# Optimization experiments

Measured on AMD Instinct MI355X. Metric: run time of the kernel, lower is better.

The kernel has to match this reference:

```python
import jax, jax.numpy as jnp
import numpy as np
import math

D_MODEL = 1024
N_HEADS = 16
D_K = D_MODEL // N_HEADS
D_FF = 4096
B, S = 2, 1024
EPS = 1e-6
MASK_FILL = 1e-9  # source uses masked_fill_(mask==0, 1e-09), NOT -inf


def layer_norm(x, alpha, bias):
    # torch: mean + unbiased std (ddof=1), normalized by (std + eps)
    mean = jnp.mean(x, axis=-1, keepdims=True)
    std = jnp.std(x, axis=-1, keepdims=True, ddof=1)
    return alpha * (x - mean) / (std + EPS) + bias


def setup_inputs() -> dict:
    key = jax.random.key(0)
    ks = jax.random.split(key, 6)
    sc = 0.02
    return {
        "x": jax.random.normal(ks[0], (B, S, D_MODEL), jnp.float32),
        "mask": jax.random.randint(ks[1], (B, 1, S, S), 0, 2, jnp.int32),
        "Wq": jax.random.normal(ks[2], (D_MODEL, D_MODEL), jnp.float32) * sc,
        "Wo": jax.random.normal(ks[3], (D_MODEL, D_MODEL), jnp.float32) * sc,
        "W1": jax.random.normal(ks[4], (D_MODEL, D_FF), jnp.float32) * sc,
        "B1": jnp.zeros((D_FF,), jnp.float32),
        "W2": jax.random.normal(ks[5], (D_FF, D_MODEL), jnp.float32) * sc,
        "B2": jnp.zeros((D_MODEL,), jnp.float32),
        "ln1_a": jnp.ones((D_MODEL,), jnp.float32),
        "ln1_b": jnp.zeros((D_MODEL,), jnp.float32),
        "ln2_a": jnp.ones((D_MODEL,), jnp.float32),
        "ln2_b": jnp.zeros((D_MODEL,), jnp.float32),
    }


def reference(x, mask, Wq, Wo, W1, B1, W2, B2, ln1_a, ln1_b, ln2_a, ln2_b):
    # --- residual 1: pre-norm self-attention ---
    n = layer_norm(x, ln1_a, ln1_b)
    # source bug preserved: Wq is applied to q, k AND v; q==k==v here
    qkv = (n @ Wq).reshape(B, S, N_HEADS, D_K).transpose(0, 2, 1, 3)  # [B,H,S,dk]
    scores = jnp.einsum('bhqd,bhkd->bhqk', qkv, qkv) / math.sqrt(D_K)
    scores = jnp.where(mask == 0, MASK_FILL, scores)
    attn = jax.nn.softmax(scores, axis=-1)
    ctx = jnp.einsum('bhqk,bhkd->bhqd', attn, qkv)
    ctx = ctx.transpose(0, 2, 1, 3).reshape(B, S, D_MODEL)
    x = x + ctx @ Wo
    # --- residual 2: pre-norm FFN ---
    n2 = layer_norm(x, ln2_a, ln2_b)
    ff = jax.nn.relu(n2 @ W1 + B1) @ W2 + B2
    return x + ff
```

## Files before the change

kernel.cpp:

```cpp
#include <hip/hip_runtime.h>
#include <hip/hip_bf16.h>
#include <stdint.h>

#define D_MODEL 1024
#define S_LEN 1024
#define BATCH 2
#define NHEADS 16
#define DK 64
#define DFF 4096

typedef __attribute__((ext_vector_type(8))) short short8;
typedef __attribute__((ext_vector_type(4))) float f32x4;

__device__ __forceinline__ unsigned short f2bf(float f) {
  union { float f; unsigned u; } v; v.f = f;
  unsigned r = v.u + 0x7FFFu + ((v.u >> 16) & 1u);
  return (unsigned short)(r >> 16);
}

__device__ __forceinline__ float bf2f(unsigned short s) {
  union { float f; unsigned u; } v; v.u = ((unsigned)s) << 16;
  return v.f;
}

__device__ __forceinline__ void gll16(const void* g, void* l) {
  __builtin_amdgcn_global_load_lds(
      (const __attribute__((address_space(1))) void*)g,
      (__attribute__((address_space(3))) void*)l, 16, 0, 0);
}

__global__ __launch_bounds__(256)
void ln_kernel(const float* __restrict__ x,
               const float* __restrict__ alpha,
               const float* __restrict__ beta,
               unsigned short* __restrict__ out) {
  const int row = blockIdx.x;
  const int tid = threadIdx.x;
  const float4 v = ((const float4*)(x + (int64_t)row * D_MODEL))[tid];
  float s = v.x + v.y + v.z + v.w;
  float ss = v.x * v.x + v.y * v.y + v.z * v.z + v.w * v.w;
  #pragma unroll
  for (int m = 32; m; m >>= 1) {
    s += __shfl_down(s, m);
    ss += __shfl_down(ss, m);
  }
  __shared__ float red[10];
  const int wave = tid >> 6;
  if ((tid & 63) == 0) { red[wave] = s; red[4 + wave] = ss; }
  __syncthreads();
  if (tid == 0) {
    float S = red[0] + red[1] + red[2] + red[3];
    float SS = red[4] + red[5] + red[6] + red[7];
    float mean = S * (1.f / 1024.f);
    float var = (SS - 1024.f * mean * mean) * (1.f / 1023.f);
    float inv = 1.f / (sqrtf(fmaxf(var, 0.f)) + 1e-6f);
    red[8] = mean; red[9] = inv;
  }
  __syncthreads();
  const float mean = red[8], inv = red[9];
  const float4 a = ((const float4*)alpha)[tid];
  const float4 bb = ((const float4*)beta)[tid];
  union { unsigned short us[4]; uint2 u2; } pk;
  pk.us[0] = f2bf(a.x * (v.x - mean) * inv + bb.x);
  pk.us[1] = f2bf(a.y * (v.y - mean) * inv + bb.y);
  pk.us[2] = f2bf(a.z * (v.z - mean) * inv + bb.z);
  pk.us[3] = f2bf(a.w * (v.w - mean) * inv + bb.w);
  ((uint2*)(out + (int64_t)row * D_MODEL))[tid] = pk.u2;
}

__global__ __launch_bounds__(256)
void wt_kernel(const float* __restrict__ W, unsigned short* __restrict__ Wt,
               int K, int N) {
  __shared__ unsigned short tile[32][33];
  const int k0 = blockIdx.y * 32, n0 = blockIdx.x * 32;
  const int tx = threadIdx.x & 31, ty = threadIdx.x >> 5;
  #pragma unroll
  for (int i = 0; i < 4; i++) {
    int r = ty + i * 8;
    tile[r][tx] = f2bf(W[(int64_t)(k0 + r) * N + n0 + tx]);
  }
  __syncthreads();
  #pragma unroll
  for (int i = 0; i < 4; i++) {
    int r = ty + i * 8;
    Wt[(int64_t)(n0 + r) * K + k0 + tx] = tile[tx][r];
  }
}

__global__ __launch_bounds__(256)
void qkvt_kernel(const unsigned short* __restrict__ qkv,
                 unsigned short* __restrict__ qkvT) {
  __shared__ unsigned short tile[32][33];
  const int s0 = blockIdx.x * 32, d0 = blockIdx.y * 32, bh = blockIdx.z;
  const int b = bh >> 4, h = bh & 15;
  const int tx = threadIdx.x & 31, ty = threadIdx.x >> 5;
  #pragma unroll
  for (int i = 0; i < 4; i++) {
    int r = ty + i * 8;
    tile[r][tx] = qkv[(int64_t)(b * S_LEN + s0 + r) * D_MODEL + h * DK + d0 + tx];
  }
  __syncthreads();
  #pragma unroll
  for (int i = 0; i < 4; i++) {
    int r = ty + i * 8;
    qkvT[(int64_t)(bh * DK + d0 + r) * S_LEN + s0 + tx] = tile[tx][r];
  }
}

__global__ __launch_bounds__(256)
void mprep_kernel(const int* __restrict__ mask, unsigned short* __restrict__ Mf) {
  const int gid = blockIdx.x * 256 + threadIdx.x;
  const int lo = gid & 15;
  const int ktb = (gid >> 4) & 31;
  const int q4 = (gid >> 9) & 255;
  const int b = gid >> 17;
  const int* mrow = mask + ((int64_t)b << 20) + (int64_t)q4 * 4096 + ktb * 32 + lo;
  union { unsigned short us[8]; short8 v; } o;
  #pragma unroll
  for (int r = 0; r < 4; r++) {
    o.us[r * 2]     = mrow[r * 1024]      ? 0x3F80 : 0;
    o.us[r * 2 + 1] = mrow[r * 1024 + 16] ? 0x3F80 : 0;
  }
  ((short8*)Mf)[gid] = o.v;
}

template<int BM, int BN, int BK, int BIAS, int RELU, int RES, int OUTBF>
__global__ __launch_bounds__(256)
void gemm_t(const unsigned short* __restrict__ A,
            const unsigned short* __restrict__ Bt,
            const float* __restrict__ bias,
            const float* __restrict__ res,
            void* __restrict__ outp,
            int M, int N, int K) {
  constexpr int NCH = BK / 8;
  constexpr int RPW = 512 / BK;
  constexpr int RPR = 2048 / BK;
  constexpr int RA = (BM * BK) / 2048;
  constexpr int RB = (BN * BK) / 2048;
  constexpr int MI = BM / 32;
  constexpr int NJ = BN / 32;
  constexpr int KK = BK / 32;

  __shared__ __align__(16) unsigned short As[BM * BK];
  __shared__ __align__(16) unsigned short Bs[BN * BK];

  const int tid = threadIdx.x;
  const int lane = tid & 63;
  const int wave = tid >> 6;
  const int lo = lane & 15, hi = lane >> 4;

  const int cpx = gridDim.x >> 3;
  const int sid = (blockIdx.x & 7) * cpx + (blockIdx.x >> 3);
  const int nbx = N / BN;
  const int n0 = (sid % nbx) * BN;
  const int m0 = (sid / nbx) * BM;
  const int wr = (wave >> 1) * (BM / 2);
  const int wc = (wave & 1) * (BN / 2);

  auto swz = [](int row, int c) -> int {
    if (BK == 128) return c ^ ((row & 7) << 1);
    if (BK == 64)  return c ^ (row & 7);
    return c ^ ((row >> 1) & 3);
  };

  const int sr = lane / NCH;
  const int sc = lane % NCH;

  f32x4 acc[MI][NJ] = {};

  for (int k0 = 0; k0 < K; k0 += BK) {
    #pragma unroll
    for (int r = 0; r < RA; r++) {
      const int row = r * RPR + wave * RPW + sr;
      gll16(A + (int64_t)(m0 + row) * K + k0 + swz(row, sc) * 8,
            &As[r * 2048 + wave * 512]);
    }
    #pragma unroll
    for (int r = 0; r < RB; r++) {
      const int row = r * RPR + wave * RPW + sr;
      gll16(Bt + (int64_t)(n0 + row) * K + k0 + swz(row, sc) * 8,
            &Bs[r * 2048 + wave * 512]);
    }
    __syncthreads();
    #pragma unroll
    for (int kk = 0; kk < KK; kk++) {
      short8 af[MI], bfr[NJ];
      #pragma unroll
      for (int t = 0; t < MI; t++) {
        const int row = wr + t * 16 + lo;
        af[t] = *(const short8*)&As[row * BK + swz(row, kk * 4 + hi) * 8];
      }
      #pragma unroll
      for (int t = 0; t < NJ; t++) {
        const int row = wc + t * 16 + lo;
        bfr[t] = *(const short8*)&Bs[row * BK + swz(row, kk * 4 + hi) * 8];
      }
      #pragma unroll
      for (int i = 0; i < MI; i++)
        #pragma unroll
        for (int j = 0; j < NJ; j++)
          acc[i][j] = __builtin_amdgcn_mfma_f32_16x16x32_bf16(af[i], bfr[j], acc[i][j], 0, 0, 0);
    }
    __syncthreads();
  }

  #pragma unroll
  for (int i = 0; i < MI; i++) {
    const int row = m0 + wr + i * 16 + hi * 4;
    #pragma unroll
    for (int j = 0; j < NJ; j++) {
      const int col = n0 + wc + j * 16 + lo;
      #pragma unroll
      for (int r = 0; r < 4; r++) {
        float v = acc[i][j][r];
        if (BIAS) v += bias[col];
        if (RELU) v = fmaxf(v, 0.f);
        if (RES)  v += res[(int64_t)(row + r) * N + col];
        if (OUTBF)
          ((unsigned short*)outp)[(int64_t)(row + r) * N + col] = f2bf(v);
        else
          ((float*)outp)[(int64_t)(row + r) * N + col] = v;
      }
    }
  }
}

__global__ __launch_bounds__(256)
void attn_kernel(const unsigned short* __restrict__ qkv,
                 const unsigned short* __restrict__ qkvT,
                 const unsigned short* __restrict__ Mf,
                 float* __restrict__ part,
                 float* __restrict__ psum) {
  __shared__ __align__(16) unsigned short Ks[64 * 64];
  __shared__ __align__(16) unsigned short Vs[64 * 64];
  __shared__ __align__(16) unsigned short Ms[512 * 8];
  __shared__ __align__(16) unsigned short Plds[4][16 * 40];
  const int tid = threadIdx.x;
  const int lane = tid & 63;
  const int wave = tid >> 6;
  const int lo = lane & 15, hi = lane >> 4;
  const int L = blockIdx.x;
  const int xcd = L & 7, idx = L >> 3;
  const int b = xcd >> 2;
  const int h = (xcd & 3) * 4 + (idx >> 5);
  const int split = (idx >> 4) & 1;
  const int qt = idx & 15;
  const int bh = b * 16 + h;
  const int q0 = qt * 64 + wave * 16;

  const unsigned short* qb =
      qkv + (int64_t)(b * S_LEN + q0 + lo) * D_MODEL + h * DK + hi * 8;
  const short8 qf0 = *(const short8*)qb;
  const short8 qf1 = *(const short8*)(qb + 32);

  f32x4 oacc[4] = {};
  float rsum[4] = {0.f, 0.f, 0.f, 0.f};
  unsigned short* Pw = Plds[wave];
  const int kbeg = split * 512;
  const int q4w = wave * 4 + hi;
  const int xr = lo & 7;

  for (int kti = 0; kti < 8; kti++) {
    const int kt = kbeg + kti * 64;
    #pragma unroll
    for (int r = 0; r < 2; r++) {
      const int c = r * 256 + tid;
      const int row = c >> 3;
      const int chg = (c & 7) ^ (row & 7);
      gll16(qkv + (int64_t)(b * S_LEN + kt + row) * D_MODEL + h * DK + chg * 8,
            &Ks[(r * 256 + wave * 64) * 8]);
      gll16(qkvT + (int64_t)(bh * DK + row) * S_LEN + kt + chg * 8,
            &Vs[(r * 256 + wave * 64) * 8]);
      const int q4l = c >> 5;
      const int u2 = (c >> 4) & 1;
      const int log = (c & 15) ^ q4l;
      gll16(Mf + ((int64_t)((b * 256 + qt * 16 + q4l) * 32 + (kt >> 5) + u2) * 16 + log) * 8,
            &Ms[(r * 256 + wave * 64) * 8]);
    }
    __syncthreads();
    #pragma unroll
    for (int u = 0; u < 2; u++) {
      const short8 kf00 = *(const short8*)&Ks[((u * 32 + lo) * 8 + (hi ^ xr)) * 8];
      const short8 kf01 = *(const short8*)&Ks[((u * 32 + lo) * 8 + ((4 + hi) ^ xr)) * 8];
      const short8 kf10 = *(const short8*)&Ks[((u * 32 + 16 + lo) * 8 + (hi ^ xr)) * 8];
      const short8 kf11 = *(const short8*)&Ks[((u * 32 + 16 + lo) * 8 + ((4 + hi) ^ xr)) * 8];
      const short8 mf = *(const short8*)&Ms[(q4w * 32 + u * 16 + (lo ^ q4w)) * 8];
      f32x4 s0 = {}, s1 = {};
      s0 = __builtin_amdgcn_mfma_f32_16x16x32_bf16(qf0, kf00, s0, 0, 0, 0);
      s0 = __builtin_amdgcn_mfma_f32_16x16x32_bf16(qf1, kf01, s0, 0, 0, 0);
      s1 = __builtin_amdgcn_mfma_f32_16x16x32_bf16(qf0, kf10, s1, 0, 0, 0);
      s1 = __builtin_amdgcn_mfma_f32_16x16x32_bf16(qf1, kf11, s1, 0, 0, 0);
      #pragma unroll
      for (int r = 0; r < 4; r++) {
        const float m0_ = bf2f((unsigned short)mf[r * 2]);
        const float m1_ = bf2f((unsigned short)mf[r * 2 + 1]);
        const float e0_ = __expf(s0[r] * 0.125f);
        const float e1_ = __expf(s1[r] * 0.125f);
        const float p0_ = fmaf(m0_, e0_ - 1.f, 1.f);
        const float p1_ = fmaf(m1_, e1_ - 1.f, 1.f);
        rsum[r] += p0_ + p1_;
        Pw[(hi * 4 + r) * 40 + lo]      = f2bf(p0_);
        Pw[(hi * 4 + r) * 40 + 16 + lo] = f2bf(p1_);
      }
      const short8 pf = *(const short8*)&Pw[lo * 40 + hi * 8];
      #pragma unroll
      for (int t = 0; t < 4; t++) {
        const short8 vf = *(const short8*)&Vs[((t * 16 + lo) * 8 + ((u * 4 + hi) ^ xr)) * 8];
        oacc[t] = __builtin_amdgcn_mfma_f32_16x16x32_bf16(pf, vf, oacc[t], 0, 0, 0);
      }
    }
    __syncthreads();
  }

  #pragma unroll
  for (int m = 1; m < 16; m <<= 1)
    #pragma unroll
    for (int r = 0; r < 4; r++) rsum[r] += __shfl_xor(rsum[r], m);

  const int64_t prow = (int64_t)(split * 32 + bh) * 1024;
  #pragma unroll
  for (int t = 0; t < 4; t++)
    #pragma unroll
    for (int r = 0; r < 4; r++)
      part[(prow + q0 + hi * 4 + r) * 64 + t * 16 + lo] = oacc[t][r];
  if (lo == 0)
    #pragma unroll
    for (int r = 0; r < 4; r++)
      psum[prow + q0 + hi * 4 + r] = rsum[r];
}

__global__ __launch_bounds__(256)
void acomb_kernel(const float* __restrict__ part,
                  const float* __restrict__ psum,
                  unsigned short* __restrict__ ctx) {
  const int idx4 = blockIdx.x * 256 + threadIdx.x;
  const int d4 = idx4 & 15;
  const int q = (idx4 >> 4) & 1023;
  const int bh = idx4 >> 14;
  const int b = bh >> 4, h = bh & 15;
  const float4* p4 = (const float4*)part;
  const float4 a0 = p4[(int64_t)(bh * 1024 + q) * 16 + d4];
  const float4 a1 = p4[524288 + (int64_t)(bh * 1024 + q) * 16 + d4];
  const float rs = psum[bh * 1024 + q] + psum[32768 + bh * 1024 + q];
  const float inv = 1.f / rs;
  union { unsigned short us[4]; uint2 u2; } pk;
  pk.us[0] = f2bf((a0.x + a1.x) * inv);
  pk.us[1] = f2bf((a0.y + a1.y) * inv);
  pk.us[2] = f2bf((a0.z + a1.z) * inv);
  pk.us[3] = f2bf((a0.w + a1.w) * inv);
  *(uint2*)(ctx + (int64_t)(b * S_LEN + q) * D_MODEL + h * DK + d4 * 4) = pk.u2;
}

extern "C" void kernel_launch(void* const* d_in, const int* in_sizes, int n_in,
                              void* d_out, int out_size, void* d_ws, size_t ws_size,
                              hipStream_t stream) {
  (void)in_sizes; (void)n_in; (void)out_size; (void)ws_size;
  const float* x    = (const float*)d_in[0];
  const int*   mask = (const int*)d_in[1];
  const float* Wq   = (const float*)d_in[2];
  const float* Wo   = (const float*)d_in[3];
  const float* W1   = (const float*)d_in[4];
  const float* B1   = (const float*)d_in[5];
  const float* W2   = (const float*)d_in[6];
  const float* B2   = (const float*)d_in[7];
  const float* ln1a = (const float*)d_in[8];
  const float* ln1b = (const float*)d_in[9];
  const float* ln2a = (const float*)d_in[10];
  const float* ln2b = (const float*)d_in[11];
  float* out = (float*)d_out;

  char* ws = (char*)d_ws;
  unsigned short* WqT  = (unsigned short*)(ws);
  unsigned short* WoT  = (unsigned short*)(ws + (2ull  << 20));
  unsigned short* W1T  = (unsigned short*)(ws + (4ull  << 20));
  unsigned short* W2T  = (unsigned short*)(ws + (12ull << 20));
  unsigned short* n1   = (unsigned short*)(ws + (20ull << 20));
  float*          psum = (float*)(ws + (20ull << 20));
  unsigned short* qkv  = (unsigned short*)(ws + (24ull << 20));
  unsigned short* qkvT = (unsigned short*)(ws + (28ull << 20));
  unsigned short* Mf   = (unsigned short*)(ws + (32ull << 20));
  unsigned short* ctx  = (unsigned short*)(ws + (32ull << 20));
  unsigned short* n2   = (unsigned short*)(ws + (36ull << 20));
  float*          part = (float*)(ws + (40ull << 20));
  unsigned short* h1   = (unsigned short*)(ws + (40ull << 20));
  float* x1 = out;

  dim3 blk(256);
  wt_kernel<<<dim3(32, 32),  blk, 0, stream>>>(Wq, WqT, 1024, 1024);
  wt_kernel<<<dim3(32, 32),  blk, 0, stream>>>(Wo, WoT, 1024, 1024);
  wt_kernel<<<dim3(128, 32), blk, 0, stream>>>(W1, W1T, 1024, 4096);
  wt_kernel<<<dim3(32, 128), blk, 0, stream>>>(W2, W2T, 4096, 1024);
  mprep_kernel<<<1024, blk, 0, stream>>>(mask, Mf);

  ln_kernel<<<2048, blk, 0, stream>>>(x, ln1a, ln1b, n1);
  gemm_t<64,64,128, 0,0,0,1><<<512, blk, 0, stream>>>(n1, WqT, nullptr, nullptr, qkv, 2048, 1024, 1024);
  qkvt_kernel<<<dim3(32, 2, 32), blk, 0, stream>>>(qkv, qkvT);
  attn_kernel<<<1024, blk, 0, stream>>>(qkv, qkvT, Mf, part, psum);
  acomb_kernel<<<2048, blk, 0, stream>>>(part, psum, ctx);
  gemm_t<64,64,128, 0,0,1,0><<<512, blk, 0, stream>>>(ctx, WoT, nullptr, x, x1, 2048, 1024, 1024);
  ln_kernel<<<2048, blk, 0, stream>>>(x1, ln2a, ln2b, n2);
  gemm_t<128,128,64, 1,1,0,1><<<512, blk, 0, stream>>>(n2, W1T, B1, nullptr, h1, 2048, 4096, 1024);
  gemm_t<64,64,128, 1,0,1,0><<<512, blk, 0, stream>>>(h1, W2T, B2, x1, out, 2048, 1024, 4096);
}
```

Measured before the change: 145.2 us.

## Double-buffer GEMM loads, split K across waves, merge weight transposes

Replaces the templated GEMM with a double-buffered variant that prefetches the next K tile during compute. For the 64x64 GEMMs each wave takes a different 32-wide K slice of the 128-wide tile, and the per-wave partial sums are combined through LDS before the epilogue. A specialized FFN1 GEMM keeps the 128x128 tile with double buffering. The four weight-transpose launches are merged into one. This aims to hide global-load latency and cut launch overhead, at the cost of doubled LDS use (lower occupancy) and an extra cross-wave reduction.

Result: slower. 495.5 us (+241.3%).

```diff
diff --git a/kernel.cpp b/kernel.cpp
--- a/kernel.cpp
+++ b/kernel.cpp
@@ -69,10 +69,18 @@
 }
 
 __global__ __launch_bounds__(256)
-void wt_kernel(const float* __restrict__ W, unsigned short* __restrict__ Wt,
-               int K, int N) {
+void wtall_kernel(const float* __restrict__ Wq, const float* __restrict__ Wo,
+                  const float* __restrict__ W1, const float* __restrict__ W2,
+                  unsigned short* __restrict__ WqT, unsigned short* __restrict__ WoT,
+                  unsigned short* __restrict__ W1T, unsigned short* __restrict__ W2T) {
   __shared__ unsigned short tile[32][33];
-  const int k0 = blockIdx.y * 32, n0 = blockIdx.x * 32;
+  int id = blockIdx.x;
+  const float* W; unsigned short* Wt; int K, N, bx, by;
+  if (id < 1024)      { W = Wq; Wt = WqT; K = 1024; N = 1024; bx = id & 31;  by = id >> 5; }
+  else if (id < 2048) { id -= 1024; W = Wo; Wt = WoT; K = 1024; N = 1024; bx = id & 31;  by = id >> 5; }
+  else if (id < 6144) { id -= 2048; W = W1; Wt = W1T; K = 1024; N = 4096; bx = id & 127; by = id >> 7; }
+  else                { id -= 6144; W = W2; Wt = W2T; K = 4096; N = 1024; bx = id & 31;  by = id >> 5; }
+  const int k0 = by * 32, n0 = bx * 32;
   const int tx = threadIdx.x & 31, ty = threadIdx.x >> 5;
   #pragma unroll
   for (int i = 0; i < 4; i++) {
@@ -124,26 +132,16 @@
   ((short8*)Mf)[gid] = o.v;
 }
 
-template<int BM, int BN, int BK, int BIAS, int RELU, int RES, int OUTBF>
-__global__ __launch_bounds__(256)
-void gemm_t(const unsigned short* __restrict__ A,
-            const unsigned short* __restrict__ Bt,
-            const float* __restrict__ bias,
-            const float* __restrict__ res,
-            void* __restrict__ outp,
-            int M, int N, int K) {
-  constexpr int NCH = BK / 8;
-  constexpr int RPW = 512 / BK;
-  constexpr int RPR = 2048 / BK;
-  constexpr int RA = (BM * BK) / 2048;
-  constexpr int RB = (BN * BK) / 2048;
-  constexpr int MI = BM / 32;
-  constexpr int NJ = BN / 32;
-  constexpr int KK = BK / 32;
-
-  __shared__ __align__(16) unsigned short As[BM * BK];
-  __shared__ __align__(16) unsigned short Bs[BN * BK];
-
+template<int BIAS, int RELU, int RES, int OUTBF>
+__global__ __launch_bounds__(256)
+void gemm_ks(const unsigned short* __restrict__ A,
+             const unsigned short* __restrict__ Bt,
+             const float* __restrict__ bias,
+             const float* __restrict__ res,
+             void* __restrict__ outp,
+             int M, int N, int K) {
+  __shared__ __align__(16) unsigned short As[2][8192];
+  __shared__ __align__(16) unsigned short Bs[2][8192];
   const int tid = threadIdx.x;
   const int lane = tid & 63;
   const int wave = tid >> 6;
@@ -151,75 +149,187 @@
 
   const int cpx = gridDim.x >> 3;
   const int sid = (blockIdx.x & 7) * cpx + (blockIdx.x >> 3);
-  const int nbx = N / BN;
-  const int n0 = (sid % nbx) * BN;
-  const int m0 = (sid / nbx) * BM;
-  const int wr = (wave >> 1) * (BM / 2);
-  const int wc = (wave & 1) * (BN / 2);
-
-  auto swz = [](int row, int c) -> int {
-    if (BK == 128) return c ^ ((row & 7) << 1);
-    if (BK == 64)  return c ^ (row & 7);
-    return c ^ ((row >> 1) & 3);
+  const int nbx = N >> 6;
+  const int n0 = (sid % nbx) << 6;
+  const int m0 = (sid / nbx) << 6;
+
+  const int sr = lane >> 4;
+  const int sc = lane & 15;
+  const int srow = wave * 4 + sr;
+  const int sch = (sc ^ (srow & 7)) * 8;
+  const unsigned short* Ag = A + (int64_t)(m0 + srow) * K + sch;
+  const unsigned short* Bg = Bt + (int64_t)(n0 + srow) * K + sch;
+
+  const int rch = ((wave * 4 + hi) ^ (lo & 7)) * 8;
+
+  f32x4 acc[4][4] = {};
+  const int NT = K >> 7;
+
+  auto stage = [&](int buf, int k0) {
+    #pragma unroll
+    for (int r = 0; r < 4; r++)
+      gll16(Ag + (int64_t)r * 16 * K + k0, &As[buf][r * 2048 + wave * 512]);
+    #pragma unroll
+    for (int r = 0; r < 4; r++)
+      gll16(Bg + (int64_t)r * 16 * K + k0, &Bs[buf][r * 2048 + wave * 512]);
   };
 
-  const int sr = lane / NCH;
-  const int sc = lane % NCH;
-
-  f32x4 acc[MI][NJ] = {};
-
-  for (int k0 = 0; k0 < K; k0 += BK) {
-    #pragma unroll
-    for (int r = 0; r < RA; r++) {
-      const int row = r * RPR + wave * RPW + sr;
-      gll16(A + (int64_t)(m0 + row) * K + k0 + swz(row, sc) * 8,
-            &As[r * 2048 + wave * 512]);
+  stage(0, 0);
+  __syncthreads();
+  int cur = 0;
+  for (int t = 0; t < NT; t++) {
+    if (t + 1 < NT) stage(cur ^ 1, (t + 1) << 7);
+    short8 af[4], bf[4];
+    #pragma unroll
+    for (int q = 0; q < 4; q++) {
+      af[q] = *(const short8*)&As[cur][(q * 16 + lo) * 128 + rch];
+      bf[q] = *(const short8*)&Bs[cur][(q * 16 + lo) * 128 + rch];
     }
     #pragma unroll
-    for (int r = 0; r < RB; r++) {
-      const int row = r * RPR + wave * RPW + sr;
-      gll16(Bt + (int64_t)(n0 + row) * K + k0 + swz(row, sc) * 8,
-            &Bs[r * 2048 + wave * 512]);
+    for (int i = 0; i < 4; i++)
+      #pragma unroll
+      for (int j = 0; j < 4; j++)
+        acc[i][j] = __builtin_amdgcn_mfma_f32_16x16x32_bf16(af[i], bf[j], acc[i][j], 0, 0, 0);
+    __syncthreads();
+    cur ^= 1;
+  }
+
+  float* red = (float*)&As[0][0];
+  if (wave >= 2) {
+    #pragma unroll
+    for (int i = 0; i < 4; i++)
+      #pragma unroll
+      for (int j = 0; j < 4; j++)
+        *(f32x4*)&red[(wave - 2) * 4096 + (i * 4 + j) * 256 + lane * 4] = acc[i][j];
+  }
+  __syncthreads();
+  if (wave < 2) {
+    #pragma unroll
+    for (int i = 0; i < 4; i++)
+      #pragma unroll
+      for (int j = 0; j < 4; j++)
+        acc[i][j] += *(const f32x4*)&red[wave * 4096 + (i * 4 + j) * 256 + lane * 4];
+  }
+  __syncthreads();
+  if (wave == 0) {
+    #pragma unroll
+    for (int i = 2; i < 4; i++)
+      #pragma unroll
+      for (int j = 0; j < 4; j++)
+        *(f32x4*)&red[((i - 2) * 4 + j) * 256 + lane * 4] = acc[i][j];
+  } else if (wave == 1) {
+    #pragma unroll
+    for (int i = 0; i < 2; i++)
+      #pragma unroll
+      for (int j = 0; j < 4; j++)
+        *(f32x4*)&red[2048 + (i * 4 + j) * 256 + lane * 4] = acc[i][j];
+  }
+  __syncthreads();
+
+  if (wave < 2) {
+    const int ib = wave * 2;
+    #pragma unroll
+    for (int ii = 0; ii < 2; ii++) {
+      const int i = ib + ii;
+      #pragma unroll
+      for (int j = 0; j < 4; j++) {
+        f32x4 v4 = acc[i][j];
+        v4 += *(const f32x4*)&red[(wave ? (ii * 4 + j) * 256 : 2048 + (i * 4 + j) * 256) + lane * 4];
+        const int row = m0 + i * 16 + hi * 4;
+        const int col = n0 + j * 16 + lo;
+        #pragma unroll
+        for (int r = 0; r < 4; r++) {
+          float v = v4[r];
+          if (BIAS) v += bias[col];
+          if (RELU) v = fmaxf(v, 0.f);
+          if (RES)  v += res[(int64_t)(row + r) * N + col];
+          if (OUTBF)
+            ((unsigned short*)outp)[(int64_t)(row + r) * N + col] = f2bf(v);
+          else
+            ((float*)outp)[(int64_t)(row + r) * N + col] = v;
+        }
+      }
+    }
+  }
+}
+
+__global__ __launch_bounds__(256)
+void gemm_ffn1(const unsigned short* __restrict__ A,
+               const unsigned short* __restrict__ Bt,
+               const float* __restrict__ bias,
+               unsigned short* __restrict__ outp,
+               int M, int N, int K) {
+  __shared__ __align__(16) unsigned short As[2][8192];
+  __shared__ __align__(16) unsigned short Bs[2][8192];
+  const int tid = threadIdx.x;
+  const int lane = tid & 63;
+  const int wave = tid >> 6;
+  const int lo = lane & 15, hi = lane >> 4;
+
+  const int cpx = gridDim.x >> 3;
+  const int sid = (blockIdx.x & 7) * cpx + (blockIdx.x >> 3);
+  const int nbx = N >> 7;
+  const int n0 = (sid % nbx) << 7;
+  const int m0 = (sid / nbx) << 7;
+  const int wr = (wave >> 1) * 64;
+  const int wc = (wave & 1) * 64;
+
+  const int sr = lane >> 3;
+  const int sc = lane & 7;
+  const int srow = wave * 8 + sr;
+  const int sch = (sc ^ (srow & 7)) * 8;
+  const unsigned short* Ag = A + (int64_t)(m0 + srow) * K + sch;
+  const unsigned short* Bg = Bt + (int64_t)(n0 + srow) * K + sch;
+
+  const int xr = lo & 7;
+
+  f32x4 acc[4][4] = {};
+  const int NT = K >> 6;
+
+  auto stage = [&](int buf, int k0) {
+    #pragma unroll
+    for (int r = 0; r < 4; r++)
+      gll16(Ag + (int64_t)r * 32 * K + k0, &As[buf][r * 2048 + wave * 512]);
+    #pragma unroll
+    for (int r = 0; r < 4; r++)
+      gll16(Bg + (int64_t)r * 32 * K + k0, &Bs[buf][r * 2048 + wave * 512]);
+  };
+
+  stage(0, 0);
+  __syncthreads();
+  int cur = 0;
+  for (int t = 0; t < NT; t++) {
+    if (t + 1 < NT) stage(cur ^ 1, (t + 1) << 6);
+    #pragma unroll
+    for (int kk = 0; kk < 2; kk++) {
+      short8 af[4], bf[4];
+      const int ch = ((kk * 4 + hi) ^ xr) * 8;
+      #pragma unroll
+      for (int q = 0; q < 4; q++) {
+        af[q] = *(const short8*)&As[cur][(wr + q * 16 + lo) * 64 + ch];
+        bf[q] = *(const short8*)&Bs[cur][(wc + q * 16 + lo) * 64 + ch];
+      }
+      #pragma unroll
+      for (int i = 0; i < 4; i++)
+        #pragma unroll
+        for (int j = 0; j < 4; j++)
+          acc[i][j] = __builtin_amdgcn_mfma_f32_16x16x32_bf16(af[i], bf[j], acc[i][j], 0, 0, 0);
     }
     __syncthreads();
-    #pragma unroll
-    for (int kk = 0; kk < KK; kk++) {
-      short8 af[MI], bfr[NJ];
-      #pragma unroll
-      for (int t = 0; t < MI; t++) {
-        const int row = wr + t * 16 + lo;
-        af[t] = *(const short8*)&As[row * BK + swz(row, kk * 4 + hi) * 8];
-      }
-      #pragma unroll
-      for (int t = 0; t < NJ; t++) {
-        const int row = wc + t * 16 + lo;
-        bfr[t] = *(const short8*)&Bs[row * BK + swz(row, kk * 4 + hi) * 8];
-      }
-      #pragma unroll
-      for (int i = 0; i < MI; i++)
-        #pragma unroll
-        for (int j = 0; j < NJ; j++)
-          acc[i][j] = __builtin_amdgcn_mfma_f32_16x16x32_bf16(af[i], bfr[j], acc[i][j], 0, 0, 0);
-    }
-    __syncthreads();
-  }
-
-  #pragma unroll
-  for (int i = 0; i < MI; i++) {
+    cur ^= 1;
+  }
+
+  #pragma unroll
+  for (int i = 0; i < 4; i++) {
     const int row = m0 + wr + i * 16 + hi * 4;
     #pragma unroll
-    for (int j = 0; j < NJ; j++) {
+    for (int j = 0; j < 4; j++) {
       const int col = n0 + wc + j * 16 + lo;
+      const float bv = bias[col];
       #pragma unroll
       for (int r = 0; r < 4; r++) {
-        float v = acc[i][j][r];
-        if (BIAS) v += bias[col];
-        if (RELU) v = fmaxf(v, 0.f);
-        if (RES)  v += res[(int64_t)(row + r) * N + col];
-        if (OUTBF)
-          ((unsigned short*)outp)[(int64_t)(row + r) * N + col] = f2bf(v);
-        else
-          ((float*)outp)[(int64_t)(row + r) * N + col] = v;
+        float v = fmaxf(acc[i][j][r] + bv, 0.f);
+        outp[(int64_t)(row + r) * N + col] = f2bf(v);
       }
     }
   }
@@ -386,19 +496,16 @@
   float* x1 = out;
 
   dim3 blk(256);
-  wt_kernel<<<dim3(32, 32),  blk, 0, stream>>>(Wq, WqT, 1024, 1024);
-  wt_kernel<<<dim3(32, 32),  blk, 0, stream>>>(Wo, WoT, 1024, 1024);
-  wt_kernel<<<dim3(128, 32), blk, 0, stream>>>(W1, W1T, 1024, 4096);
-  wt_kernel<<<dim3(32, 128), blk, 0, stream>>>(W2, W2T, 4096, 1024);
+  wtall_kernel<<<10240, blk, 0, stream>>>(Wq, Wo, W1, W2, WqT, WoT, W1T, W2T);
   mprep_kernel<<<1024, blk, 0, stream>>>(mask, Mf);
 
   ln_kernel<<<2048, blk, 0, stream>>>(x, ln1a, ln1b, n1);
-  gemm_t<64,64,128, 0,0,0,1><<<512, blk, 0, stream>>>(n1, WqT, nullptr, nullptr, qkv, 2048, 1024, 1024);
+  gemm_ks<0,0,0,1><<<512, blk, 0, stream>>>(n1, WqT, nullptr, nullptr, qkv, 2048, 1024, 1024);
   qkvt_kernel<<<dim3(32, 2, 32), blk, 0, stream>>>(qkv, qkvT);
   attn_kernel<<<1024, blk, 0, stream>>>(qkv, qkvT, Mf, part, psum);
   acomb_kernel<<<2048, blk, 0, stream>>>(part, psum, ctx);
-  gemm_t<64,64,128, 0,0,1,0><<<512, blk, 0, stream>>>(ctx, WoT, nullptr, x, x1, 2048, 1024, 1024);
+  gemm_ks<0,0,1,0><<<512, blk, 0, stream>>>(ctx, WoT, nullptr, x, x1, 2048, 1024, 1024);
   ln_kernel<<<2048, blk, 0, stream>>>(x1, ln2a, ln2b, n2);
-  gemm_t<128,128,64, 1,1,0,1><<<512, blk, 0, stream>>>(n2, W1T, B1, nullptr, h1, 2048, 4096, 1024);
-  gemm_t<64,64,128, 1,0,1,0><<<512, blk, 0, stream>>>(h1, W2T, B2, x1, out, 2048, 1024, 4096);
-}
+  gemm_ffn1<<<512, blk, 0, stream>>>(n2, W1T, B1, h1, 2048, 4096, 1024);
+  gemm_ks<1,0,1,0><<<512, blk, 0, stream>>>(h1, W2T, B2, x1, out, 2048, 1024, 4096);
+}
```

## Double-buffer GEMM shared-memory tiles and merge weight transposes into one launch

Applied to the files above, without the earlier changes.

The GEMM kernel now uses two LDS buffers, issuing the global-to-LDS loads for the next K tile while MFMAs run on the current one, so there is one barrier per tile instead of two. BK is halved for each GEMM so LDS use stays roughly the same, and the load-address math is precomputed per thread. The four weight-transpose launches become one kernel that picks its matrix from the block index, which cuts launch overhead. The smaller BK doubles the number of loop iterations and barriers, and the unrolled pair loop assumes an even tile count.

After: 166.1 us. 1.14x slower.

```diff
diff --git a/kernel.cpp b/kernel.cpp
--- a/kernel.cpp
+++ b/kernel.cpp
@@ -69,10 +69,18 @@
 }
 
 __global__ __launch_bounds__(256)
-void wt_kernel(const float* __restrict__ W, unsigned short* __restrict__ Wt,
-               int K, int N) {
+void wtall_kernel(const float* __restrict__ Wq, const float* __restrict__ Wo,
+                  const float* __restrict__ W1, const float* __restrict__ W2,
+                  unsigned short* __restrict__ WqT, unsigned short* __restrict__ WoT,
+                  unsigned short* __restrict__ W1T, unsigned short* __restrict__ W2T) {
   __shared__ unsigned short tile[32][33];
-  const int k0 = blockIdx.y * 32, n0 = blockIdx.x * 32;
+  int id = blockIdx.x;
+  const float* W; unsigned short* Wt; int K, N, bx, by;
+  if (id < 1024)      { W = Wq; Wt = WqT; K = 1024; N = 1024; bx = id & 31;  by = id >> 5; }
+  else if (id < 2048) { id -= 1024; W = Wo; Wt = WoT; K = 1024; N = 1024; bx = id & 31;  by = id >> 5; }
+  else if (id < 6144) { id -= 2048; W = W1; Wt = W1T; K = 1024; N = 4096; bx = id & 127; by = id >> 7; }
+  else                { id -= 6144; W = W2; Wt = W2T; K = 4096; N = 1024; bx = id & 31;  by = id >> 5; }
+  const int k0 = by * 32, n0 = bx * 32;
   const int tx = threadIdx.x & 31, ty = threadIdx.x >> 5;
   #pragma unroll
   for (int i = 0; i < 4; i++) {
@@ -126,23 +134,21 @@
 
 template<int BM, int BN, int BK, int BIAS, int RELU, int RES, int OUTBF>
 __global__ __launch_bounds__(256)
-void gemm_t(const unsigned short* __restrict__ A,
-            const unsigned short* __restrict__ Bt,
-            const float* __restrict__ bias,
-            const float* __restrict__ res,
-            void* __restrict__ outp,
-            int M, int N, int K) {
+void gemm_db(const unsigned short* __restrict__ A,
+             const unsigned short* __restrict__ Bt,
+             const float* __restrict__ bias,
+             const float* __restrict__ res,
+             void* __restrict__ outp,
+             int M, int N, int K) {
   constexpr int NCH = BK / 8;
-  constexpr int RPW = 512 / BK;
-  constexpr int RPR = 2048 / BK;
   constexpr int RA = (BM * BK) / 2048;
   constexpr int RB = (BN * BK) / 2048;
   constexpr int MI = BM / 32;
   constexpr int NJ = BN / 32;
   constexpr int KK = BK / 32;
 
-  __shared__ __align__(16) unsigned short As[BM * BK];
-  __shared__ __align__(16) unsigned short Bs[BN * BK];
+  __shared__ __align__(16) unsigned short As[2][BM * BK];
+  __shared__ __align__(16) unsigned short Bs[2][BN * BK];
 
   const int tid = threadIdx.x;
   const int lane = tid & 63;
@@ -158,49 +164,70 @@
   const int wc = (wave & 1) * (BN / 2);
 
   auto swz = [](int row, int c) -> int {
-    if (BK == 128) return c ^ ((row & 7) << 1);
-    if (BK == 64)  return c ^ (row & 7);
+    if (BK >= 64) return c ^ (row & 7);
     return c ^ ((row >> 1) & 3);
   };
 
-  const int sr = lane / NCH;
-  const int sc = lane % NCH;
+  const unsigned short* Ap[RA];
+  const unsigned short* Bp[RB];
+  #pragma unroll
+  for (int r = 0; r < RA; r++) {
+    const int c = r * 256 + tid;
+    const int row = c / NCH, sc = c % NCH;
+    Ap[r] = A + (int64_t)(m0 + row) * K + swz(row, sc) * 8;
+  }
+  #pragma unroll
+  for (int r = 0; r < RB; r++) {
+    const int c = r * 256 + tid;
+    const int row = c / NCH, sc = c % NCH;
+    Bp[r] = Bt + (int64_t)(n0 + row) * K + swz(row, sc) * 8;
+  }
 
   f32x4 acc[MI][NJ] = {};
-
-  for (int k0 = 0; k0 < K; k0 += BK) {
-    #pragma unroll
-    for (int r = 0; r < RA; r++) {
-      const int row = r * RPR + wave * RPW + sr;
-      gll16(A + (int64_t)(m0 + row) * K + k0 + swz(row, sc) * 8,
-            &As[r * 2048 + wave * 512]);
-    }
-    #pragma unroll
-    for (int r = 0; r < RB; r++) {
-      const int row = r * RPR + wave * RPW + sr;
-      gll16(Bt + (int64_t)(n0 + row) * K + k0 + swz(row, sc) * 8,
-            &Bs[r * 2048 + wave * 512]);
-    }
-    __syncthreads();
+  const int NT = K / BK;
+
+  auto stage = [&](unsigned short* Al, unsigned short* Bl, int k0) {
+    #pragma unroll
+    for (int r = 0; r < RA; r++)
+      gll16(Ap[r] + k0, Al + (r * 256 + wave * 64) * 8);
+    #pragma unroll
+    for (int r = 0; r < RB; r++)
+      gll16(Bp[r] + k0, Bl + (r * 256 + wave * 64) * 8);
+  };
+
+  auto compute = [&](const unsigned short* Al, const unsigned short* Bl) {
     #pragma unroll
     for (int kk = 0; kk < KK; kk++) {
-      short8 af[MI], bfr[NJ];
+      short8 af[MI], bf[NJ];
       #pragma unroll
       for (int t = 0; t < MI; t++) {
         const int row = wr + t * 16 + lo;
-        af[t] = *(const short8*)&As[row * BK + swz(row, kk * 4 + hi) * 8];
+        af[t] = *(const short8*)&Al[row * BK + swz(row, kk * 4 + hi) * 8];
       }
       #pragma unroll
       for (int t = 0; t < NJ; t++) {
         const int row = wc + t * 16 + lo;
-        bfr[t] = *(const short8*)&Bs[row * BK + swz(row, kk * 4 + hi) * 8];
+        bf[t] = *(const short8*)&Bl[row * BK + swz(row, kk * 4 + hi) * 8];
       }
       #pragma unroll
       for (int i = 0; i < MI; i++)
         #pragma unroll
         for (int j = 0; j < NJ; j++)
-          acc[i][j] = __builtin_amdgcn_mfma_f32_16x16x32_bf16(af[i], bfr[j], acc[i][j], 0, 0, 0);
+          acc[i][j] = __builtin_amdgcn_mfma_f32_16x16x32_bf16(af[i], bf[j], acc[i][j], 0, 0, 0);
     }
+  };
+
+  unsigned short* A0 = &As[0][0]; unsigned short* B0 = &Bs[0][0];
+  unsigned short* A1 = &As[1][0]; unsigned short* B1 = &Bs[1][0];
+
+  stage(A0, B0, 0);
+  __syncthreads();
+  for (int t = 0; t < NT; t += 2) {
+    stage(A1, B1, (t + 1) * BK);
+    compute(A0, B0);
+    __syncthreads();
+    if (t + 2 < NT) stage(A0, B0, (t + 2) * BK);
+    compute(A1, B1);
     __syncthreads();
   }
 
@@ -386,19 +413,16 @@
   float* x1 = out;
 
   dim3 blk(256);
-  wt_kernel<<<dim3(32, 32),  blk, 0, stream>>>(Wq, WqT, 1024, 1024);
-  wt_kernel<<<dim3(32, 32),  blk, 0, stream>>>(Wo, WoT, 1024, 1024);
-  wt_kernel<<<dim3(128, 32), blk, 0, stream>>>(W1, W1T, 1024, 4096);
-  wt_kernel<<<dim3(32, 128), blk, 0, stream>>>(W2, W2T, 4096, 1024);
+  wtall_kernel<<<10240, blk, 0, stream>>>(Wq, Wo, W1, W2, WqT, WoT, W1T, W2T);
   mprep_kernel<<<1024, blk, 0, stream>>>(mask, Mf);
 
   ln_kernel<<<2048, blk, 0, stream>>>(x, ln1a, ln1b, n1);
-  gemm_t<64,64,128, 0,0,0,1><<<512, blk, 0, stream>>>(n1, WqT, nullptr, nullptr, qkv, 2048, 1024, 1024);
+  gemm_db<64,64,64, 0,0,0,1><<<512, blk, 0, stream>>>(n1, WqT, nullptr, nullptr, qkv, 2048, 1024, 1024);
   qkvt_kernel<<<dim3(32, 2, 32), blk, 0, stream>>>(qkv, qkvT);
   attn_kernel<<<1024, blk, 0, stream>>>(qkv, qkvT, Mf, part, psum);
   acomb_kernel<<<2048, blk, 0, stream>>>(part, psum, ctx);
-  gemm_t<64,64,128, 0,0,1,0><<<512, blk, 0, stream>>>(ctx, WoT, nullptr, x, x1, 2048, 1024, 1024);
+  gemm_db<64,64,64, 0,0,1,0><<<512, blk, 0, stream>>>(ctx, WoT, nullptr, x, x1, 2048, 1024, 1024);
   ln_kernel<<<2048, blk, 0, stream>>>(x1, ln2a, ln2b, n2);
-  gemm_t<128,128,64, 1,1,0,1><<<512, blk, 0, stream>>>(n2, W1T, B1, nullptr, h1, 2048, 4096, 1024);
-  gemm_t<64,64,128, 1,0,1,0><<<512, blk, 0, stream>>>(h1, W2T, B2, x1, out, 2048, 1024, 4096);
-}
+  gemm_db<128,128,32, 1,1,0,1><<<512, blk, 0, stream>>>(n2, W1T, B1, nullptr, h1, 2048, 4096, 1024);
+  gemm_db<64,64,64, 1,0,1,0><<<512, blk, 0, stream>>>(h1, W2T, B2, x1, out, 2048, 1024, 4096);
+}
```
